# Performance work log

Measured on AMD Instinct MI355X. Metric: run time of the kernel, lower is better.

The kernel has to match this reference:

```python
import jax, jax.numpy as jnp
import numpy as np

B, C, H, W = 2, 64, 128, 128
K, SCALE, NUM_RES = 3, 2, 2
KK = K * K


def conv(x, w, b, pad=0):
    y = jax.lax.conv_general_dilated(x, w, (1, 1), [(pad, pad), (pad, pad)],
                                     dimension_numbers=('NCHW', 'OIHW', 'NCHW'))
    return y + b[None, :, None, None]


def unfold_dilated(x, k, d):
    # mimics nn.Unfold(kernel_size=k, dilation=d, padding=(k//2)*d) -> (b, c, k*k, h, w)
    pad = (k // 2) * d
    b, c, h, w = x.shape
    xp = jnp.pad(x, ((0, 0), (0, 0), (pad, pad), (pad, pad)))
    slices = [xp[:, :, i * d:i * d + h, j * d:j * d + w]
              for i in range(k) for j in range(k)]
    return jnp.stack(slices, axis=2)


def setup_inputs() -> dict:
    key = jax.random.key(0)
    ks = jax.random.split(key, 32)
    def p(k, shape, s=0.05):
        return jax.random.normal(k, shape, dtype=jnp.float32) * s
    H2, W2 = H * SCALE, W * SCALE
    return {
        'depth':  p(ks[0], (B, C, H2, W2), 1.0),
        'guide':  p(ks[1], (B, C, H2, W2), 1.0),
        'inputs': p(ks[2], (B, C, H, W), 1.0),
        # depth_kernel branch: 1x1 C->C (ReLU), 1x1 C->k^2
        'dk_w1': p(ks[3], (C, C, 1, 1)), 'dk_b1': jnp.zeros((C,), jnp.float32),
        'dk_w2': p(ks[4], (KK, C, 1, 1)), 'dk_b2': jnp.zeros((KK,), jnp.float32),
        # guide_kernel branch
        'gk_w1': p(ks[5], (C, C, 1, 1)), 'gk_b1': jnp.zeros((C,), jnp.float32),
        'gk_w2': p(ks[6], (KK, C, 1, 1)), 'gk_b2': jnp.zeros((KK,), jnp.float32),
        # weight_net: 3x3 2C->C (ReLU), 3x3 C->C (ReLU, TUnet stand-in), 3x3 C->1
        'wn_w1': p(ks[7], (C, 2 * C, 3, 3)), 'wn_b1': jnp.zeros((C,), jnp.float32),
        'wn_w2': p(ks[8], (C, C, 3, 3)), 'wn_b2': jnp.zeros((C,), jnp.float32),
        'wn_w3': p(ks[9], (1, C, 3, 3)), 'wn_b3': jnp.zeros((1,), jnp.float32),
        # residual blocks on inputs: NUM_RES x (conv3x3-ReLU-conv3x3 + skip)
        'rb_w': p(ks[10], (NUM_RES, 2, C, C, 3, 3)),
        'rb_b': jnp.zeros((NUM_RES, 2, C), jnp.float32),
        'aff_scale': 0.5 * KK * jnp.ones((1,), jnp.float32),
    }


def reference(depth, guide, inputs,
              dk_w1, dk_b1, dk_w2, dk_b2,
              gk_w1, gk_b1, gk_w2, gk_b2,
              wn_w1, wn_b1, wn_w2, wn_b2, wn_w3, wn_b3,
              rb_w, rb_b, aff_scale):
    # weight map
    wm = jax.nn.relu(conv(jnp.concatenate([depth, guide], axis=1), wn_w1, wn_b1, 1))
    wm = jax.nn.relu(conv(wm, wn_w2, wn_b2, 1))
    weight_map = conv(wm, wn_w3, wn_b3, 1)                       # (b,1,h_,w_)
    # per-pixel kernels
    dk = conv(jax.nn.relu(conv(depth, dk_w1, dk_b1)), dk_w2, dk_b2)
    gk = conv(jax.nn.relu(conv(guide, gk_w1, gk_b1)), gk_w2, gk_b2)
    dk = jax.nn.softmax(dk, axis=1)
    gk = jax.nn.softmax(gk, axis=1)
    fuse = weight_map * dk + (1.0 - weight_map) * gk
    fuse = jnp.tanh(fuse) / (aff_scale + 1e-8)
    ksum = jnp.maximum(jnp.sum(jnp.abs(fuse), axis=1, keepdims=True) + 1e-4, 1.0)
    fuse = fuse / ksum                                            # (b,k^2,h_,w_)
    # residual conv stack on low-res inputs
    x = inputs
    for i in range(NUM_RES):
        r = jax.nn.relu(conv(x, rb_w[i, 0], rb_b[i, 0], 1))
        r = conv(r, rb_w[i, 1], rb_b[i, 1], 1)
        x = x + r
    b, c, h, w = x.shape
    up = jax.image.resize(x, (b, c, h * SCALE, w * SCALE), method='bilinear')
    unf = unfold_dilated(up, K, SCALE)                            # (b,c,k^2,h_,w_)
    out = jnp.einsum('bkhw,bckhw->bchw', fuse, unf)
    return out
```

## Files before the change

kernel.cpp:

```cpp
#include <hip/hip_runtime.h>
#include <hip/hip_bf16.h>
#include <math.h>

#define HW2 (256*256)
#define HW1 (128*128)

typedef __attribute__((ext_vector_type(8))) short short8;
typedef __attribute__((ext_vector_type(4))) float floatx4;

__device__ __forceinline__ float b2f(ushort u) {
    union { unsigned int i; float f; } v; v.i = ((unsigned int)u) << 16; return v.f;
}
__device__ __forceinline__ ushort f2b(float f) {
    __hip_bfloat16 h = __float2bfloat16(f); return *(ushort*)&h;
}
__device__ __forceinline__ float fast_tanh(float x) {
    float cx = fminf(fmaxf(x, -15.f), 15.f);
    float t = __expf(2.f * cx);
    return (t - 1.f) / (t + 1.f);
}

__global__ __launch_bounds__(256)
void repack_all(const float* __restrict__ wn_w1, const float* __restrict__ wn_w2,
                const float* __restrict__ rb_w,
                const float* __restrict__ dk_w1, const float* __restrict__ gk_w1,
                const float* __restrict__ dk_w2, const float* __restrict__ gk_w2,
                const float* __restrict__ wn_w3,
                ushort* __restrict__ wt_wn1, ushort* __restrict__ wt_wn2,
                ushort* __restrict__ wt_rb,
                ushort* __restrict__ w1d, ushort* __restrict__ w1g,
                ushort* __restrict__ w2d, ushort* __restrict__ w2g,
                ushort* __restrict__ wt3) {
    int idx = blockIdx.x * 256 + threadIdx.x;
    int role = blockIdx.y;
    if (role == 0) {
        if (idx >= 73728) return;
        int o = idx / 1152; int rem = idx - o * 1152;
        int ci = rem / 9;   int t = rem - ci * 9;
        wt_wn1[(((size_t)(ci >> 5) * 9 + t) * 64 + o) * 32 + (ci & 31)] = f2b(wn_w1[idx]);
    } else if (role <= 5) {
        if (idx >= 36864) return;
        const float* w = (role == 1) ? wn_w2 : rb_w + (size_t)(role - 2) * 36864;
        ushort* wt     = (role == 1) ? wt_wn2 : wt_rb + (size_t)(role - 2) * 36864;
        int o = idx / 576; int rem = idx - o * 576;
        int ci = rem / 9;  int t = rem - ci * 9;
        wt[(((size_t)(ci >> 5) * 9 + t) * 64 + o) * 32 + (ci & 31)] = f2b(w[idx]);
    } else if (role == 6) {
        if (idx >= 10240) return;
        if (idx < 4096)      w1d[idx] = f2b(dk_w1[idx]);
        else if (idx < 8192) w1g[idx - 4096] = f2b(gk_w1[idx - 4096]);
        else if (idx < 9216) { int i = idx - 8192; w2d[i] = (i >> 6) < 9 ? f2b(dk_w2[i]) : (ushort)0; }
        else                 { int i = idx - 9216; w2g[i] = (i >> 6) < 9 ? f2b(gk_w2[i]) : (ushort)0; }
    } else {
        if (idx >= 9216) return;
        int kc = idx / 512; int rem = idx - kc * 512;
        int n = rem >> 5, c = rem & 31;
        int cc = kc / 9, t = kc - cc * 9;
        wt3[idx] = (n == 0) ? f2b(wn_w3[(cc * 32 + c) * 9 + t]) : (ushort)0;
    }
}

__global__ __launch_bounds__(256)
void to_chunked(const float* __restrict__ in, ushort* __restrict__ outc,
                int H, int W, int Cchunks) {
    int P = W + 2, Q = H + 2;
    int plane_px = P * Q;
    int idx = blockIdx.x * 256 + threadIdx.x;
    if (idx >= plane_px) return;
    int py = idx / P, px = idx - py * P;
    int bc = blockIdx.y;
    int b = bc / Cchunks, cc = bc - b * Cchunks;
    ushort* dst = outc + ((size_t)bc * plane_px + idx) * 32;
    short8* d8 = (short8*)dst;
    if (py == 0 || py == Q - 1 || px == 0 || px == P - 1) {
        short8 z = (short8){0, 0, 0, 0, 0, 0, 0, 0};
        d8[0] = z; d8[1] = z; d8[2] = z; d8[3] = z;
        return;
    }
    int y = py - 1, x = px - 1;
    const float* src = in + ((size_t)b * (Cchunks * 32) + cc * 32) * H * W
                          + (size_t)y * W + x;
    ushort tmp[32];
#pragma unroll
    for (int c = 0; c < 32; ++c)
        tmp[c] = f2b(src[(size_t)c * H * W]);
#pragma unroll
    for (int v = 0; v < 4; ++v) d8[v] = *(short8*)&tmp[v * 8];
}

__global__ __launch_bounds__(256)
void to_chunked_hi(const float* __restrict__ depth, const float* __restrict__ guide,
                   ushort* __restrict__ outc) {
    const int P = 258;
    int plane_px = P * P;
    int idx = blockIdx.x * 256 + threadIdx.x;
    if (idx >= plane_px) return;
    int py = idx / P, px = idx - py * P;
    int pl = blockIdx.y;
    const float* srcb = (pl < 4) ? depth : guide;
    int bc = pl & 3;
    int b = bc >> 1, cc = bc & 1;
    ushort* dst = outc + ((size_t)pl * plane_px + idx) * 32;
    short8* d8 = (short8*)dst;
    if (py == 0 || py == P - 1 || px == 0 || px == P - 1) {
        short8 z = (short8){0, 0, 0, 0, 0, 0, 0, 0};
        d8[0] = z; d8[1] = z; d8[2] = z; d8[3] = z;
        return;
    }
    int y = py - 1, x = px - 1;
    const float* src = srcb + ((size_t)b * 64 + cc * 32) * HW2 + (size_t)y * 256 + x;
    ushort tmp[32];
#pragma unroll
    for (int c = 0; c < 32; ++c)
        tmp[c] = f2b(src[(size_t)c * HW2]);
#pragma unroll
    for (int v = 0; v < 4; ++v) d8[v] = *(short8*)&tmp[v * 8];
}

__global__ __launch_bounds__(256)
void zero_border2(ushort* __restrict__ buf256, ushort* __restrict__ buf128) {
    int region = blockIdx.y;
    int H = region ? 128 : 256;
    int P = H + 2, Q = H + 2;
    ushort* buf = region ? buf128 : buf256;
    int nb = 2 * P + 2 * H;
    int idx = blockIdx.x * 256 + threadIdx.x;
    if (idx >= nb * 8) return;
    int pl = idx / nb, r = idx - pl * nb;
    int py, px;
    if (r < P)          { py = 0;     px = r; }
    else if (r < 2 * P) { py = Q - 1; px = r - P; }
    else { int k = r - 2 * P; py = 1 + (k >> 1); px = (k & 1) ? P - 1 : 0; }
    ushort* dst = buf + ((size_t)pl * P * Q + (size_t)py * P + px) * 32;
    short8 z = (short8){0, 0, 0, 0, 0, 0, 0, 0};
    short8* d8 = (short8*)dst;
    d8[0] = z; d8[1] = z; d8[2] = z; d8[3] = z;
}

template<int NCHUNK, int ROWS, bool RELU, bool HAS_SKIP, bool CONCAT2>
__global__ __launch_bounds__(256, 2)
void conv3x3_reg(const ushort* __restrict__ inA, const ushort* __restrict__ inB,
                 const ushort* __restrict__ wt, const float* __restrict__ bias,
                 const ushort* __restrict__ skip, ushort* __restrict__ outc,
                 int H, int W) {
    const int P = W + 2;
    const size_t plane = (size_t)P * (H + 2) * 32;
    int tid = threadIdx.x;
    int wv = tid >> 6, lane = tid & 63, ml = lane & 15, q = lane >> 4;
    int x0 = blockIdx.x * 16;
    int rowsPerBlock = (blockDim.x >> 6) * ROWS;
    int yb = blockIdx.y * rowsPerBlock + wv * ROWS;
    int b = blockIdx.z;

    floatx4 acc[ROWS][4];
#pragma unroll
    for (int r = 0; r < ROWS; ++r)
#pragma unroll
        for (int n = 0; n < 4; ++n) acc[r][n] = (floatx4){0.f, 0.f, 0.f, 0.f};

    for (int cc = 0; cc < NCHUNK; ++cc) {
        const ushort* base;
        if (CONCAT2) {
            constexpr int HC = NCHUNK / 2;
            if (cc < HC) base = inA + ((size_t)(b * HC + cc)) * plane;
            else         base = inB + ((size_t)(b * HC + cc - HC)) * plane;
        } else {
            base = inA + ((size_t)(b * NCHUNK + cc)) * plane;
        }
        const ushort* wb = wt + (size_t)cc * 18432;
#pragma unroll
        for (int dy = 0; dy < 3; ++dy) {
            short8 afr[3][ROWS], bfr[3][4];
#pragma unroll
            for (int dx = 0; dx < 3; ++dx) {
#pragma unroll
                for (int r = 0; r < ROWS; ++r)
                    afr[dx][r] = *(const short8*)&base[((size_t)(yb + r + dy) * P
                                                       + (x0 + ml + dx)) * 32 + q * 8];
#pragma unroll
                for (int n = 0; n < 4; ++n)
                    bfr[dx][n] = *(const short8*)&wb[(size_t)((dy * 3 + dx) * 64
                                                              + n * 16 + ml) * 32 + q * 8];
            }
#pragma unroll
            for (int dx = 0; dx < 3; ++dx)
#pragma unroll
                for (int r = 0; r < ROWS; ++r)
#pragma unroll
                    for (int n = 0; n < 4; ++n)
                        acc[r][n] = __builtin_amdgcn_mfma_f32_16x16x32_bf16(
                            afr[dx][r], bfr[dx][n], acc[r][n], 0, 0, 0);
        }
    }

#pragma unroll
    for (int r = 0; r < ROWS; ++r) {
        int y = yb + r;
#pragma unroll
        for (int n = 0; n < 4; ++n) {
            int ch = n * 16 + ml;
            int occ = ch >> 5, ocl = ch & 31;
            float bs = bias[ch];
            size_t pbase = ((size_t)(b * 2 + occ)) * plane + ((size_t)(y + 1) * P) * 32 + ocl;
#pragma unroll
            for (int e = 0; e < 4; ++e) {
                int x = x0 + q * 4 + e;
                float v = acc[r][n][e] + bs;
                if (RELU) v = fmaxf(v, 0.f);
                if (HAS_SKIP)
                    v += b2f(skip[((size_t)(b * 2 + occ)) * plane
                                  + ((size_t)(y + 1) * P + (x + 1)) * 32 + ocl]);
                outc[pbase + (size_t)(x + 1) * 32] = f2b(v);
            }
        }
    }
}

__global__ __launch_bounds__(256, 2)
void kernels_fuse_mfma(const ushort* __restrict__ depth_c, const ushort* __restrict__ guide_c,
                       const ushort* __restrict__ bufB,
                       const ushort* __restrict__ wt3, const float* __restrict__ wn_b3,
                       const ushort* __restrict__ w1d, const float* __restrict__ b1d,
                       const ushort* __restrict__ w2d, const float* __restrict__ b2d,
                       const ushort* __restrict__ w1g, const float* __restrict__ b1g,
                       const ushort* __restrict__ w2g, const float* __restrict__ b2g,
                       const float* __restrict__ aff, float* __restrict__ fuse_out) {
    __shared__ __align__(16) ushort hid[2][4][16 * 72];
    __shared__ float wmv[4][16];

    int tid = threadIdx.x;
    int wv = tid >> 6, lane = tid & 63, ml = lane & 15, q = lane >> 4;
    int p0 = blockIdx.x * 64 + wv * 16;
    int b = p0 >> 16, rem0 = p0 & 65535;
    const size_t plane = (size_t)258 * 258 * 32;

    int rem = rem0 + ml;
    int y = rem >> 8, x = rem & 255;
    size_t poff = ((size_t)(y + 1) * 258 + (x + 1)) * 32;

    short8 afr[2][2];
#pragma unroll
    for (int kc = 0; kc < 2; ++kc) {
        afr[0][kc] = *(const short8*)&depth_c[(size_t)(b * 2 + kc) * plane + poff + q * 8];
        afr[1][kc] = *(const short8*)&guide_c[(size_t)(b * 2 + kc) * plane + poff + q * 8];
    }
    const ushort* bb0 = bufB + (size_t)(b * 2 + 0) * plane;
    const ushort* bb1 = bufB + (size_t)(b * 2 + 1) * plane;
    short8 a30[9], a31[9];
#pragma unroll
    for (int t = 0; t < 9; ++t) {
        int dy = t / 3, dx = t - 3 * dy;
        size_t o = ((size_t)(y + dy) * 258 + (x + dx)) * 32 + q * 8;
        a30[t] = *(const short8*)&bb0[o];
        a31[t] = *(const short8*)&bb1[o];
    }

    floatx4 acc[2][4];
#pragma unroll
    for (int br = 0; br < 2; ++br)
#pragma unroll
        for (int nt = 0; nt < 4; ++nt) acc[br][nt] = (floatx4){0.f, 0.f, 0.f, 0.f};
#pragma unroll
    for (int nt = 0; nt < 4; ++nt)
#pragma unroll
        for (int kc = 0; kc < 2; ++kc) {
            short8 bD = *(const short8*)&w1d[(size_t)((nt * 16 + ml) * 64 + kc * 32 + q * 8)];
            short8 bG = *(const short8*)&w1g[(size_t)((nt * 16 + ml) * 64 + kc * 32 + q * 8)];
            acc[0][nt] = __builtin_amdgcn_mfma_f32_16x16x32_bf16(afr[0][kc], bD, acc[0][nt], 0, 0, 0);
            acc[1][nt] = __builtin_amdgcn_mfma_f32_16x16x32_bf16(afr[1][kc], bG, acc[1][nt], 0, 0, 0);
        }

    floatx4 dw[4];
#pragma unroll
    for (int u = 0; u < 4; ++u) dw[u] = (floatx4){0.f, 0.f, 0.f, 0.f};
#pragma unroll
    for (int t = 0; t < 9; ++t) {
        short8 b3 = *(const short8*)&wt3[(size_t)(t * 512 + ml * 32 + q * 8)];
        dw[t & 3] = __builtin_amdgcn_mfma_f32_16x16x32_bf16(a30[t], b3, dw[t & 3], 0, 0, 0);
    }
#pragma unroll
    for (int t = 0; t < 9; ++t) {
        short8 b3 = *(const short8*)&wt3[(size_t)((9 + t) * 512 + ml * 32 + q * 8)];
        dw[t & 3] = __builtin_amdgcn_mfma_f32_16x16x32_bf16(a31[t], b3, dw[t & 3], 0, 0, 0);
    }
    floatx4 dwm = (dw[0] + dw[1]) + (dw[2] + dw[3]);
    if (ml == 0) {
#pragma unroll
        for (int e = 0; e < 4; ++e) wmv[wv][q * 4 + e] = dwm[e];
    }

#pragma unroll
    for (int br = 0; br < 2; ++br) {
        const float* b1 = br ? b1g : b1d;
        ushort* h = hid[br][wv];
#pragma unroll
        for (int nt = 0; nt < 4; ++nt) {
            float bs = b1[nt * 16 + ml];
#pragma unroll
            for (int e = 0; e < 4; ++e) {
                float v = acc[br][nt][e] + bs;
                v = fmaxf(v, 0.f);
                h[(q * 4 + e) * 72 + nt * 16 + ml] = f2b(v);
            }
        }
    }

    floatx4 d2[2];
    d2[0] = (floatx4){0.f, 0.f, 0.f, 0.f};
    d2[1] = (floatx4){0.f, 0.f, 0.f, 0.f};
#pragma unroll
    for (int kc = 0; kc < 2; ++kc) {
        short8 a2d = *(const short8*)&w2d[(size_t)(ml * 64 + kc * 32 + q * 8)];
        short8 a2g = *(const short8*)&w2g[(size_t)(ml * 64 + kc * 32 + q * 8)];
        short8 hfd = *(const short8*)&hid[0][wv][ml * 72 + kc * 32 + q * 8];
        short8 hfg = *(const short8*)&hid[1][wv][ml * 72 + kc * 32 + q * 8];
        d2[0] = __builtin_amdgcn_mfma_f32_16x16x32_bf16(a2d, hfd, d2[0], 0, 0, 0);
        d2[1] = __builtin_amdgcn_mfma_f32_16x16x32_bf16(a2g, hfg, d2[1], 0, 0, 0);
    }

    float wm = wmv[wv][ml] + wn_b3[0];

    float sm[2][4];
#pragma unroll
    for (int br = 0; br < 2; ++br) {
        const float* b2 = br ? b2g : b2d;
        float lg[4];
#pragma unroll
        for (int e = 0; e < 4; ++e) {
            int j = q * 4 + e;
            lg[e] = (j < 9) ? (d2[br][e] + b2[j]) : -1e30f;
        }
        float m = fmaxf(fmaxf(lg[0], lg[1]), fmaxf(lg[2], lg[3]));
        m = fmaxf(m, __shfl_xor(m, 16));
        m = fmaxf(m, __shfl_xor(m, 32));
        float s = 0.f;
#pragma unroll
        for (int e = 0; e < 4; ++e) { lg[e] = __expf(lg[e] - m); s += lg[e]; }
        s += __shfl_xor(s, 16);
        s += __shfl_xor(s, 32);
        float inv = 1.f / s;
#pragma unroll
        for (int e = 0; e < 4; ++e) sm[br][e] = lg[e] * inv;
    }

    float inv_av = 1.f / (aff[0] + 1e-8f);
    float f[4];
    float s = 0.f;
#pragma unroll
    for (int e = 0; e < 4; ++e) {
        float v = wm * sm[0][e] + (1.f - wm) * sm[1][e];
        v = fast_tanh(v) * inv_av;
        f[e] = v;
        s += fabsf(v);
    }
    s += __shfl_xor(s, 16);
    s += __shfl_xor(s, 32);
    float ksum = s + 1e-4f;
    if (ksum < 1.f) ksum = 1.f;
    float invk = 1.f / ksum;
#pragma unroll
    for (int e = 0; e < 4; ++e) {
        int j = q * 4 + e;
        if (j < 9)
            fuse_out[((size_t)b * 9 + j) * HW2 + rem0 + ml] = f[e] * invk;
    }
}

__global__ __launch_bounds__(256)
void fuse_apply_up(const float* __restrict__ fuse, const ushort* __restrict__ r2c,
                   float* __restrict__ out) {
    int p = blockIdx.x * 256 + threadIdx.x;
    int pl = blockIdx.y;
    int b = pl >> 1, cc = pl & 1;
    int y = p >> 8, x = p & 255;

    int my = y >> 1, mx = x >> 1;
    float wyA = (y & 1) ? 0.75f : 0.25f;  float wyB = 1.f - wyA;
    float wxA = (x & 1) ? 0.75f : 0.25f;  float wxB = 1.f - wxA;
    int R0y = my + ((y & 1) ? 0 : -1) - 1;
    int R0x = mx + ((x & 1) ? 0 : -1) - 1;

    const float* f = fuse + (size_t)b * 9 * HW2 + p;
    float coef[4][4];
#pragma unroll
    for (int k = 0; k < 4; ++k)
#pragma unroll
        for (int l = 0; l < 4; ++l) coef[k][l] = 0.f;

#pragma unroll
    for (int ty = 0; ty < 3; ++ty) {
        int yp = y + (ty - 1) * 2;
        if (yp < 0 || yp > 255) continue;
#pragma unroll
        for (int tx = 0; tx < 3; ++tx) {
            int xp = x + (tx - 1) * 2;
            if (xp < 0 || xp > 255) continue;
            float fv = f[(size_t)(ty * 3 + tx) * HW2];
            coef[ty][tx]         += fv * wyA * wxA;
            coef[ty][tx + 1]     += fv * wyA * wxB;
            coef[ty + 1][tx]     += fv * wyB * wxA;
            coef[ty + 1][tx + 1] += fv * wyB * wxB;
        }
    }

    const ushort* base = r2c + (size_t)pl * 130 * 130 * 32;
    float acc[32];
#pragma unroll
    for (int c = 0; c < 32; ++c) acc[c] = 0.f;
#pragma unroll
    for (int k = 0; k < 4; ++k) {
        int ry = R0y + k; ry = ry < 0 ? 0 : (ry > 127 ? 127 : ry);
#pragma unroll
        for (int l = 0; l < 4; ++l) {
            int rx = R0x + l; rx = rx < 0 ? 0 : (rx > 127 ? 127 : rx);
            float cf = coef[k][l];
            const ushort* u = base + ((size_t)(ry + 1) * 130 + (rx + 1)) * 32;
#pragma unroll
            for (int c = 0; c < 32; ++c) acc[c] = fmaf(cf, b2f(u[c]), acc[c]);
        }
    }
    float* ob = out + ((size_t)(b * 64 + cc * 32)) * HW2 + p;
#pragma unroll
    for (int c = 0; c < 32; ++c) ob[(size_t)c * HW2] = acc[c];
}

extern "C" void kernel_launch(void* const* d_in, const int* in_sizes, int n_in,
                              void* d_out, int out_size, void* d_ws, size_t ws_size,
                              hipStream_t stream) {
    const float* depth  = (const float*)d_in[0];
    const float* guide  = (const float*)d_in[1];
    const float* inputs = (const float*)d_in[2];
    const float* dk_w1  = (const float*)d_in[3];
    const float* dk_b1  = (const float*)d_in[4];
    const float* dk_w2  = (const float*)d_in[5];
    const float* dk_b2  = (const float*)d_in[6];
    const float* gk_w1  = (const float*)d_in[7];
    const float* gk_b1  = (const float*)d_in[8];
    const float* gk_w2  = (const float*)d_in[9];
    const float* gk_b2  = (const float*)d_in[10];
    const float* wn_w1  = (const float*)d_in[11];
    const float* wn_b1  = (const float*)d_in[12];
    const float* wn_w2  = (const float*)d_in[13];
    const float* wn_b2  = (const float*)d_in[14];
    const float* wn_w3  = (const float*)d_in[15];
    const float* wn_b3  = (const float*)d_in[16];
    const float* rb_w   = (const float*)d_in[17];
    const float* rb_b   = (const float*)d_in[18];
    const float* aff    = (const float*)d_in[19];
    float* out = (float*)d_out;

    float* ws = (float*)d_ws;
    size_t off = 0;
    const size_t CH256 = 4260096;
    const size_t CH128 = 1081600;
    ushort* depth_c = (ushort*)(ws + off); off += CH256;
    ushort* guide_c = (ushort*)(ws + off); off += CH256;
    ushort* bufA    = (ushort*)(ws + off); off += CH256;
    ushort* bufB    = (ushort*)(ws + off); off += CH256;
    ushort* inp_c   = (ushort*)(ws + off); off += CH128;
    ushort* r0      = (ushort*)(ws + off); off += CH128;
    ushort* r1      = (ushort*)(ws + off); off += CH128;
    ushort* r2      = (ushort*)(ws + off); off += CH128;
    float* fuse     = ws + off; off += 1179648;
    ushort* wt_wn1  = (ushort*)(ws + off); off += 36864;
    ushort* wt_wn2  = (ushort*)(ws + off); off += 18432;
    ushort* wt_rb   = (ushort*)(ws + off); off += 73728;
    ushort* w1d_b   = (ushort*)(ws + off); off += 2048;
    ushort* w1g_b   = (ushort*)(ws + off); off += 2048;
    ushort* w2d_b   = (ushort*)(ws + off); off += 512;
    ushort* w2g_b   = (ushort*)(ws + off); off += 512;
    ushort* wt3_b   = (ushort*)(ws + off); off += 4608;

    repack_all<<<dim3(288, 8), 256, 0, stream>>>(
        wn_w1, wn_w2, rb_w, dk_w1, gk_w1, dk_w2, gk_w2, wn_w3,
        wt_wn1, wt_wn2, wt_rb, w1d_b, w1g_b, w2d_b, w2g_b, wt3_b);

    to_chunked_hi<<<dim3(261, 8), 256, 0, stream>>>(depth, guide, depth_c);
    to_chunked<<<dim3(67, 4), 256, 0, stream>>>(inputs, inp_c, 128, 128, 2);

    zero_border2<<<dim3(33, 2), 256, 0, stream>>>(bufA, r0);

    conv3x3_reg<4, 4, true, false, true ><<<dim3(16, 16, 2), 256, 0, stream>>>(
        depth_c, guide_c, wt_wn1, wn_b1, nullptr, bufA, 256, 256);
    conv3x3_reg<2, 4, true, false, false><<<dim3(16, 16, 2), 256, 0, stream>>>(
        bufA, nullptr, wt_wn2, wn_b2, nullptr, bufB, 256, 256);

    kernels_fuse_mfma<<<2048, 256, 0, stream>>>(depth_c, guide_c, bufB,
                                                wt3_b, wn_b3,
                                                w1d_b, dk_b1, w2d_b, dk_b2,
                                                w1g_b, gk_b1, w2g_b, gk_b2,
                                                aff, fuse);

    conv3x3_reg<2, 2, true,  false, false><<<dim3(8, 16, 2), 256, 0, stream>>>(
        inp_c, nullptr, wt_rb + 0 * 36864, rb_b + 0 * 64, nullptr, r0, 128, 128);
    conv3x3_reg<2, 2, false, true,  false><<<dim3(8, 16, 2), 256, 0, stream>>>(
        r0, nullptr, wt_rb + 1 * 36864, rb_b + 1 * 64, inp_c, r1, 128, 128);
    conv3x3_reg<2, 2, true,  false, false><<<dim3(8, 16, 2), 256, 0, stream>>>(
        r1, nullptr, wt_rb + 2 * 36864, rb_b + 2 * 64, nullptr, r0, 128, 128);
    conv3x3_reg<2, 2, false, true,  false><<<dim3(8, 16, 2), 256, 0, stream>>>(
        r0, nullptr, wt_rb + 3 * 36864, rb_b + 3 * 64, r1, r2, 128, 128);

    fuse_apply_up<<<dim3(256, 4), 256, 0, stream>>>(fuse, r2, out);
}
```

Measured before the change: 329.8 us.

## Vectorize hi-res chunking and stage 3x3 halo via global_load_lds

The hi-res layout conversion now has each thread load float4 runs (4 pixels × 32 channels) instead of one scalar per pixel. The padded border is no longer written inside that kernel; it is zeroed by an extended border-zeroing kernel that takes a third buffer. In the fuse kernel, the 3×3 neighbourhood of bufB for the weight-map conv is staged once per block into LDS with direct global-to-LDS loads, replacing 18 redundant per-lane global loads. This adds about 25 KB of LDS per block and a block barrier, which may reduce occupancy.

```diff
diff --git a/kernel.cpp b/kernel.cpp
--- a/kernel.cpp
+++ b/kernel.cpp
@@ -1,6 +1,7 @@
 #include <hip/hip_runtime.h>
 #include <hip/hip_bf16.h>
 #include <math.h>
+#include <stdint.h>
 
 #define HW2 (256*256)
 #define HW1 (128*128)
@@ -18,6 +19,12 @@
     float cx = fminf(fmaxf(x, -15.f), 15.f);
     float t = __expf(2.f * cx);
     return (t - 1.f) / (t + 1.f);
+}
+__device__ __forceinline__ void gload_lds16(const void* g, void* l) {
+    __builtin_amdgcn_global_load_lds(
+        (__attribute__((address_space(1))) void*)(uintptr_t)g,
+        (__attribute__((address_space(3))) void*)(unsigned)(uintptr_t)l,
+        16, 0, 0);
 }
 
 __global__ __launch_bounds__(256)
@@ -89,40 +96,41 @@
 }
 
 __global__ __launch_bounds__(256)
-void to_chunked_hi(const float* __restrict__ depth, const float* __restrict__ guide,
-                   ushort* __restrict__ outc) {
-    const int P = 258;
-    int plane_px = P * P;
-    int idx = blockIdx.x * 256 + threadIdx.x;
-    if (idx >= plane_px) return;
-    int py = idx / P, px = idx - py * P;
-    int pl = blockIdx.y;
+void to_chunked_hi4(const float* __restrict__ depth, const float* __restrict__ guide,
+                    ushort* __restrict__ outc) {
+    int gid = blockIdx.x * 256 + threadIdx.x;
+    int g   = gid & 63;
+    int y   = (gid >> 6) & 255;
+    int pl  = gid >> 14;
     const float* srcb = (pl < 4) ? depth : guide;
     int bc = pl & 3;
     int b = bc >> 1, cc = bc & 1;
-    ushort* dst = outc + ((size_t)pl * plane_px + idx) * 32;
-    short8* d8 = (short8*)dst;
-    if (py == 0 || py == P - 1 || px == 0 || px == P - 1) {
-        short8 z = (short8){0, 0, 0, 0, 0, 0, 0, 0};
-        d8[0] = z; d8[1] = z; d8[2] = z; d8[3] = z;
-        return;
-    }
-    int y = py - 1, x = px - 1;
-    const float* src = srcb + ((size_t)b * 64 + cc * 32) * HW2 + (size_t)y * 256 + x;
-    ushort tmp[32];
-#pragma unroll
-    for (int c = 0; c < 32; ++c)
-        tmp[c] = f2b(src[(size_t)c * HW2]);
-#pragma unroll
-    for (int v = 0; v < 4; ++v) d8[v] = *(short8*)&tmp[v * 8];
+    const float* src = srcb + ((size_t)b * 64 + cc * 32) * HW2 + (size_t)y * 256 + g * 4;
+    ushort tmp[4][32];
+#pragma unroll
+    for (int c = 0; c < 32; ++c) {
+        floatx4 v = *(const floatx4*)&src[(size_t)c * HW2];
+        tmp[0][c] = f2b(v[0]); tmp[1][c] = f2b(v[1]);
+        tmp[2][c] = f2b(v[2]); tmp[3][c] = f2b(v[3]);
+    }
+    ushort* dst = outc + ((size_t)pl * 258 * 258 + (size_t)(y + 1) * 258 + (g * 4 + 1)) * 32;
+#pragma unroll
+    for (int p = 0; p < 4; ++p) {
+        short8* d8 = (short8*)(dst + (size_t)p * 32);
+        d8[0] = *(short8*)&tmp[p][0];
+        d8[1] = *(short8*)&tmp[p][8];
+        d8[2] = *(short8*)&tmp[p][16];
+        d8[3] = *(short8*)&tmp[p][24];
+    }
 }
 
 __global__ __launch_bounds__(256)
-void zero_border2(ushort* __restrict__ buf256, ushort* __restrict__ buf128) {
+void zero_border3(ushort* __restrict__ buf256, ushort* __restrict__ buf128,
+                  ushort* __restrict__ bufhi) {
     int region = blockIdx.y;
-    int H = region ? 128 : 256;
+    int H = (region == 1) ? 128 : 256;
     int P = H + 2, Q = H + 2;
-    ushort* buf = region ? buf128 : buf256;
+    ushort* buf = (region == 0) ? buf256 : (region == 1) ? buf128 : bufhi;
     int nb = 2 * P + 2 * H;
     int idx = blockIdx.x * 256 + threadIdx.x;
     if (idx >= nb * 8) return;
@@ -225,6 +233,7 @@
                        const ushort* __restrict__ w1g, const float* __restrict__ b1g,
                        const ushort* __restrict__ w2g, const float* __restrict__ b2g,
                        const float* __restrict__ aff, float* __restrict__ fuse_out) {
+    __shared__ __align__(16) ushort stage[12672];
     __shared__ __align__(16) ushort hid[2][4][16 * 72];
     __shared__ float wmv[4][16];
 
@@ -238,22 +247,32 @@
     int y = rem >> 8, x = rem & 255;
     size_t poff = ((size_t)(y + 1) * 258 + (x + 1)) * 32;
 
+    int pb  = blockIdx.x * 64;
+    int y0  = (pb & 65535) >> 8;
+    int x0b = pb & 255;
+
     short8 afr[2][2];
 #pragma unroll
     for (int kc = 0; kc < 2; ++kc) {
         afr[0][kc] = *(const short8*)&depth_c[(size_t)(b * 2 + kc) * plane + poff + q * 8];
         afr[1][kc] = *(const short8*)&guide_c[(size_t)(b * 2 + kc) * plane + poff + q * 8];
     }
-    const ushort* bb0 = bufB + (size_t)(b * 2 + 0) * plane;
-    const ushort* bb1 = bufB + (size_t)(b * 2 + 1) * plane;
-    short8 a30[9], a31[9];
-#pragma unroll
-    for (int t = 0; t < 9; ++t) {
-        int dy = t / 3, dx = t - 3 * dy;
-        size_t o = ((size_t)(y + dy) * 258 + (x + dx)) * 32 + q * 8;
-        a30[t] = *(const short8*)&bb0[o];
-        a31[t] = *(const short8*)&bb1[o];
-    }
+
+    const ushort* bbase = bufB + (size_t)(b * 2) * plane;
+#pragma unroll
+    for (int i = 0; i < 7; ++i) {
+        int wofs = i * 4096 + (wv << 10);
+        int ofs  = wofs + (lane << 4);
+        if (ofs < 25344) {
+            int seg = ofs / 4224;
+            int within = ofs - seg * 4224;
+            int cc2 = seg / 3, r = seg - cc2 * 3;
+            const ushort* gsrc = bbase + (size_t)cc2 * plane
+                               + ((size_t)(y0 + r) * 258 + x0b) * 32 + (within >> 1);
+            gload_lds16(gsrc, (char*)stage + wofs);
+        }
+    }
+    __syncthreads();
 
     floatx4 acc[2][4];
 #pragma unroll
@@ -270,18 +289,23 @@
             acc[1][nt] = __builtin_amdgcn_mfma_f32_16x16x32_bf16(afr[1][kc], bG, acc[1][nt], 0, 0, 0);
         }
 
+    int colb = (wv << 4) + ml;
     floatx4 dw[4];
 #pragma unroll
     for (int u = 0; u < 4; ++u) dw[u] = (floatx4){0.f, 0.f, 0.f, 0.f};
 #pragma unroll
     for (int t = 0; t < 9; ++t) {
+        int dy2 = t / 3, dx2 = t - 3 * dy2;
+        short8 a0 = *(const short8*)&stage[(size_t)(dy2 * 66 + colb + dx2) * 32 + q * 8];
         short8 b3 = *(const short8*)&wt3[(size_t)(t * 512 + ml * 32 + q * 8)];
-        dw[t & 3] = __builtin_amdgcn_mfma_f32_16x16x32_bf16(a30[t], b3, dw[t & 3], 0, 0, 0);
+        dw[t & 3] = __builtin_amdgcn_mfma_f32_16x16x32_bf16(a0, b3, dw[t & 3], 0, 0, 0);
     }
 #pragma unroll
     for (int t = 0; t < 9; ++t) {
+        int dy2 = t / 3, dx2 = t - 3 * dy2;
+        short8 a1 = *(const short8*)&stage[(size_t)((3 + dy2) * 66 + colb + dx2) * 32 + q * 8];
         short8 b3 = *(const short8*)&wt3[(size_t)((9 + t) * 512 + ml * 32 + q * 8)];
-        dw[t & 3] = __builtin_amdgcn_mfma_f32_16x16x32_bf16(a31[t], b3, dw[t & 3], 0, 0, 0);
+        dw[t & 3] = __builtin_amdgcn_mfma_f32_16x16x32_bf16(a1, b3, dw[t & 3], 0, 0, 0);
     }
     floatx4 dwm = (dw[0] + dw[1]) + (dw[2] + dw[3]);
     if (ml == 0) {
@@ -475,10 +499,10 @@
         wn_w1, wn_w2, rb_w, dk_w1, gk_w1, dk_w2, gk_w2, wn_w3,
         wt_wn1, wt_wn2, wt_rb, w1d_b, w1g_b, w2d_b, w2g_b, wt3_b);
 
-    to_chunked_hi<<<dim3(261, 8), 256, 0, stream>>>(depth, guide, depth_c);
+    to_chunked_hi4<<<512, 256, 0, stream>>>(depth, guide, depth_c);
     to_chunked<<<dim3(67, 4), 256, 0, stream>>>(inputs, inp_c, 128, 128, 2);
 
-    zero_border2<<<dim3(33, 2), 256, 0, stream>>>(bufA, r0);
+    zero_border3<<<dim3(33, 3), 256, 0, stream>>>(bufA, r0, depth_c);
 
     conv3x3_reg<4, 4, true, false, true ><<<dim3(16, 16, 2), 256, 0, stream>>>(
         depth_c, guide_c, wt_wn1, wn_b1, nullptr, bufA, 256, 256);
```

New measurement: 327.9 us. About the same (-0.6%).
